# Kernel optimization log

Measured on AMD Instinct MI355X. Metric: run time of the kernel, lower is better.

Reference implementation:

```python
import jax, jax.numpy as jnp
import numpy as np

STRIDES = [(2, 2), (3, 3), (4, 4)]
EPS = 1e-5


def _conv1x1(x, w, b):
    # x: [B,C,H,W], w: [O,C] -> [B,O,H,W]
    return jnp.einsum('bchw,oc->bohw', x, w) + b[None, :, None, None]


def _stitch(x, hs, ws):
    # x: [B,dk,H,W] -> patches [B, hs*ws, dk*oh*ow]; patch index = i*ws + j matches
    # torch.stack over itertools.product(range(hs), range(ws)) of x[:,:,i::hs,j::ws]
    b, dk, H, W = x.shape
    oh, ow = H // hs, W // ws
    p = x.reshape(b, dk, oh, hs, ow, ws).transpose(0, 3, 5, 1, 2, 4)  # [B,hs,ws,dk,oh,ow]
    return p.reshape(b, hs * ws, dk * oh * ow)


def _unstitch(y, b, dk, hs, ws, oh, ow):
    # faithful to the torch permute(0,3,1,4,2,5): H is assembled as (hs, oh), W as (ws, ow)
    y = y.reshape(b, hs, ws, dk, oh, ow).transpose(0, 3, 1, 4, 2, 5)  # [B,dk,hs,oh,ws,ow]
    return y.reshape(b, dk, hs * oh, ws * ow)


def _attention(q, k, v):
    d = q.shape[-1]
    scores = jnp.einsum('bpd,bqd->bpq', q, k) / jnp.sqrt(jnp.asarray(d, q.dtype))
    p = jax.nn.softmax(scores, axis=-1)
    return jnp.einsum('bpq,bqd->bpd', p, v)


def _forward(x, wq, bq, wk, bk, wv, bv, w_out, b_out, gamma, beta):
    b, c, h, w = x.shape
    n = len(STRIDES)
    dk = c // n
    q = _conv1x1(x, wq, bq)
    k = _conv1x1(x, wk, bk)
    v = _conv1x1(x, wv, bv)
    outs = []
    for idx, (ws_, hs_) in enumerate(STRIDES):
        sl = slice(idx * dk, (idx + 1) * dk)
        oh, ow = h // hs_, w // ws_
        qp = _stitch(q[:, sl], hs_, ws_)
        kp = _stitch(k[:, sl], hs_, ws_)
        vp = _stitch(v[:, sl], hs_, ws_)
        y = _attention(qp, kp, vp)  # [B, hs*ws, dk*oh*ow]
        outs.append(_unstitch(y, b, dk, hs_, ws_, oh, ow))
    out = jnp.concatenate(outs, axis=1)  # [B,C,H,W]
    # output_linear: Conv3x3 -> BatchNorm2d (training-mode batch stats) -> LeakyReLU(0.2)
    y = jax.lax.conv_general_dilated(out, w_out, (1, 1), 'SAME',
                                     dimension_numbers=('NCHW', 'OIHW', 'NCHW'))
    y = y + b_out[None, :, None, None]
    mean = jnp.mean(y, axis=(0, 2, 3), keepdims=True)
    var = jnp.var(y, axis=(0, 2, 3), keepdims=True)
    y = (y - mean) * jax.lax.rsqrt(var + EPS)
    y = y * gamma[None, :, None, None] + beta[None, :, None, None]
    return jnp.where(y >= 0, y, 0.2 * y)


def setup_inputs() -> dict:
    key = jax.random.key(0)
    ks = jax.random.split(key, 10)
    B, C, H, W = 16, 192, 96, 96
    s = 0.02
    return {
        'x': jax.random.normal(ks[0], (B, C, H, W), jnp.float32),
        'wq': jax.random.normal(ks[1], (C, C), jnp.float32) * s,
        'bq': jnp.zeros((C,), jnp.float32),
        'wk': jax.random.normal(ks[2], (C, C), jnp.float32) * s,
        'bk': jnp.zeros((C,), jnp.float32),
        'wv': jax.random.normal(ks[3], (C, C), jnp.float32) * s,
        'bv': jnp.zeros((C,), jnp.float32),
        'w_out': jax.random.normal(ks[4], (C, C, 3, 3), jnp.float32) * s,
        'b_out': jnp.zeros((C,), jnp.float32),
        'gamma': jnp.ones((C,), jnp.float32),
        'beta': jnp.zeros((C,), jnp.float32),
    }


def reference(x, wq, bq, wk, bk, wv, bv, w_out, b_out, gamma, beta):
    return _forward(x, wq, bq, wk, bk, wv, bv, w_out, b_out, gamma, beta)
```

## Files before the change

### kernel.cpp

```cpp
#include <hip/hip_runtime.h>
#include <hip/hip_bf16.h>

#define BB 16
#define CC 192
#define HH 96
#define WWW 96
#define HWSZ 9216
#define DKC 64

typedef __hip_bfloat16 bf16;
typedef __attribute__((ext_vector_type(8))) short s8v;
typedef __attribute__((ext_vector_type(4))) float f32x4;

__device__ __forceinline__ float bf2f(unsigned short u) {
  union { unsigned int i; float f; } x; x.i = ((unsigned int)u) << 16; return x.f;
}
__device__ __forceinline__ unsigned short f2bf(float f) {
  union { __hip_bfloat16 h; unsigned short u; } c; c.h = __float2bfloat16(f); return c.u;
}

__global__ __launch_bounds__(256) void prep_w_kernel(const float* __restrict__ w_out,
                                                     unsigned short* __restrict__ wb9T) {
  int e = blockIdx.x * 256 + threadIdx.x;
  if (e >= 9 * CC * CC) return;
  int c = e % CC;
  int oc = (e / CC) % CC;
  int sh = e / (CC * CC);
  wb9T[e] = f2bf(w_out[((size_t)(oc * CC + c)) * 9 + sh]);
}

__global__ __launch_bounds__(256) void prep_wqkv_kernel(
    const float* __restrict__ wq, const float* __restrict__ wk, const float* __restrict__ wv,
    unsigned short* __restrict__ wqkv) {
  int e = blockIdx.x * 256 + threadIdx.x;
  if (e >= 3 * CC * CC) return;
  int sel = e / (CC * CC), r = e % (CC * CC);
  const float* w = sel == 0 ? wq : sel == 1 ? wk : wv;
  wqkv[e] = f2bf(w[r]);
}

__global__ __launch_bounds__(256) void xcvt_kernel(const float* __restrict__ x,
                                                   unsigned short* __restrict__ xb) {
  __shared__ float xt[CC][65];
  int b = blockIdx.x / 144, tile = blockIdx.x % 144;
  int pix0 = tile * 64;
  const float* xsrc = x + (size_t)b * CC * HWSZ + pix0;
  for (int e = threadIdx.x; e < CC * 16; e += 256) {
    int c = e >> 4, seg = e & 15;
    float4 t4 = *(const float4*)(xsrc + (size_t)c * HWSZ + seg * 4);
    xt[c][seg * 4 + 0] = t4.x; xt[c][seg * 4 + 1] = t4.y;
    xt[c][seg * 4 + 2] = t4.z; xt[c][seg * 4 + 3] = t4.w;
  }
  __syncthreads();
  unsigned short* dst = xb + ((size_t)(b * HWSZ + pix0)) * CC;
  for (int e = threadIdx.x; e < 24 * 64; e += 256) {
    int cg = e >> 6, p = e & 63;
    uint4 ov;
    unsigned short* ou = (unsigned short*)&ov;
    #pragma unroll
    for (int j = 0; j < 8; ++j) ou[j] = f2bf(xt[cg * 8 + j][p]);
    *(uint4*)(dst + (size_t)p * CC + cg * 8) = ov;
  }
}

#define VTS 232
__global__ __launch_bounds__(256) void qkv_mfma_kernel(
    const unsigned short* __restrict__ xb, const unsigned short* __restrict__ wqkv,
    const float* __restrict__ bq, const float* __restrict__ bk, const float* __restrict__ bv,
    unsigned short* __restrict__ q, unsigned short* __restrict__ k,
    unsigned short* __restrict__ v) {
  __shared__ unsigned short xl[96 * 200];
  __shared__ unsigned short vt[48 * VTS];
  const int tid = threadIdx.x;
  const int bid = (blockIdx.x & 7) * 192 + (blockIdx.x >> 3);
  const int h = bid % HH;
  const int b = bid / HH;
  const int lane = tid & 63, wid = tid >> 6;
  const int lr = lane & 15, hi8 = (lane >> 4) * 8, rowb = (lane >> 4) * 4;
  const int n0 = wid * 48;
  const unsigned short* xrow = xb + ((size_t)(b * HWSZ + h * WWW)) * CC;

  #pragma unroll
  for (int i = 0; i < 9; ++i) {
    int u = tid + i * 256;
    int pix = u / 24, cg = u % 24;
    *(uint4*)(xl + pix * 200 + cg * 8) = *(const uint4*)(xrow + (size_t)pix * CC + cg * 8);
  }
  __syncthreads();

  for (int sel = 0; sel < 3; ++sel) {
    const unsigned short* wsel = wqkv + (size_t)sel * CC * CC;
    f32x4 acc[6][3];
    #pragma unroll
    for (int mt = 0; mt < 6; ++mt)
      #pragma unroll
      for (int nt = 0; nt < 3; ++nt) acc[mt][nt] = (f32x4){0.f, 0.f, 0.f, 0.f};

    auto loadB = [&](int ck, s8v (&dst)[3]) {
      const unsigned short* src = wsel + ck * 32 + hi8;
      #pragma unroll
      for (int nt = 0; nt < 3; ++nt)
        dst[nt] = *(const s8v*)(src + (size_t)(n0 + nt * 16 + lr) * CC);
    };
    auto loadA = [&](int ck, s8v (&dst)[6]) {
      #pragma unroll
      for (int mt = 0; mt < 6; ++mt)
        dst[mt] = *(const s8v*)(xl + (mt * 16 + lr) * 200 + ck * 32 + hi8);
    };
    auto qstep = [&](int ck, s8v (&slot)[3], s8v (&acur)[6], s8v (&anxt)[6]) {
      if (ck < 5) loadA(ck + 1, anxt);
      #pragma unroll
      for (int mt = 0; mt < 6; ++mt)
        #pragma unroll
        for (int nt = 0; nt < 3; ++nt)
          acc[mt][nt] = __builtin_amdgcn_mfma_f32_16x16x32_bf16(acur[mt], slot[nt], acc[mt][nt], 0, 0, 0);
      if (ck + 3 < 6) loadB(ck + 3, slot);
    };

    s8v br0[3], br1[3], br2[3], aA[6], aB[6];
    loadB(0, br0); loadB(1, br1); loadB(2, br2);
    loadA(0, aA);
    qstep(0, br0, aA, aB);
    qstep(1, br1, aB, aA);
    qstep(2, br2, aA, aB);
    qstep(3, br0, aB, aA);
    qstep(4, br1, aA, aB);
    qstep(5, br2, aB, aA);

    const float* bsel = (sel == 0 ? bq : sel == 1 ? bk : bv);
    float bias[3];
    #pragma unroll
    for (int nt = 0; nt < 3; ++nt) bias[nt] = bsel[n0 + nt * 16 + lr];
    unsigned short* dst = (sel == 0 ? q : sel == 1 ? k : v) + ((size_t)(b * HWSZ + h * WWW)) * CC;
    #pragma unroll
    for (int pass = 0; pass < 2; ++pass) {
      __syncthreads();
      #pragma unroll
      for (int mt2 = 0; mt2 < 3; ++mt2)
        #pragma unroll
        for (int nt = 0; nt < 3; ++nt)
          #pragma unroll
          for (int i = 0; i < 4; ++i)
            vt[(mt2 * 16 + rowb + i) * VTS + n0 + nt * 16 + lr] =
                f2bf(acc[pass * 3 + mt2][nt][i] + bias[nt]);
      __syncthreads();
      for (int e = tid; e < 48 * 24; e += 256) {
        int p = e % 48, cg = e / 48;
        *(uint4*)(dst + (size_t)(pass * 48 + p) * CC + cg * 8) = *(uint4*)(vt + p * VTS + cg * 8);
      }
    }
  }
}

template <int HS, int WS, int OH, int OW, int IDX>
__global__ __launch_bounds__(256) void scores_kernel(
    const unsigned short* __restrict__ q, const unsigned short* __restrict__ k,
    float* __restrict__ scores) {
  constexpr int P = HS * WS;
  constexpr int PAIRS = P * P;
  constexpr int NB = 16;
  constexpr int NSUB = (256 / PAIRS) < 1 ? 1 : (256 / PAIRS);
  __shared__ float qt[128][P + 1];
  __shared__ float kt[128][P + 1];
  int b = blockIdx.x / NB;
  int blk = blockIdx.x % NB;
  const unsigned short* qb = q + (size_t)b * HWSZ * CC;
  const unsigned short* kb = k + (size_t)b * HWSZ * CC;
  int pr = threadIdx.x % PAIRS;
  int sub = threadIdx.x / PAIRS;
  int pi = pr / P, qi = pr % P;
  float acc = 0.f;
  for (int rs0 = blk * 2; rs0 < OH * OW; rs0 += NB * 2) {
    if (threadIdx.x < 16 * P) {
      int cg = threadIdx.x & 7;
      int t2 = threadIdx.x >> 3;
      int pp = t2 % P, rs2 = t2 / P;
      int rs = rs0 + rs2;
      int r = rs / OW, s = rs % OW;
      int i = pp / WS, j = pp % WS;
      int pixel = (r * HS + i) * WWW + s * WS + j;
      uint4 qv = *(const uint4*)(qb + (size_t)pixel * CC + IDX * 64 + cg * 8);
      uint4 kv = *(const uint4*)(kb + (size_t)pixel * CC + IDX * 64 + cg * 8);
      const unsigned short* qu = (const unsigned short*)&qv;
      const unsigned short* ku = (const unsigned short*)&kv;
      #pragma unroll
      for (int m = 0; m < 8; ++m) {
        qt[rs2 * 64 + cg * 8 + m][pp] = bf2f(qu[m]);
        kt[rs2 * 64 + cg * 8 + m][pp] = bf2f(ku[m]);
      }
    }
    __syncthreads();
    if (sub < NSUB) {
      #pragma unroll 4
      for (int pos = sub; pos < 128; pos += NSUB)
        acc += qt[pos][pi] * kt[pos][qi];
    }
    __syncthreads();
  }
  if (sub < NSUB) atomicAdd(scores + ((IDX * BB + b) * 256 + pr), acc);
}

__global__ void softmax_kernel(const float* __restrict__ scores, float* __restrict__ probs) {
  int t = threadIdx.x;
  int idx, b, p, P; float scale;
  if (t < 64)       { idx = 0; b = t >> 2;           p = t & 3;         P = 4;  scale = 1.f / 384.f; }
  else if (t < 208) { int u = t - 64;  idx = 1; b = u / 9;  p = u % 9;  P = 9;  scale = 1.f / 256.f; }
  else if (t < 464) { int u = t - 208; idx = 2; b = u >> 4; p = u & 15; P = 16; scale = 1.f / 192.f; }
  else return;
  const float* row = scores + (idx * BB + b) * 256 + p * P;
  float* orow = probs + (idx * BB + b) * 256 + p * P;
  float vals[16];
  float m = -1e30f;
  for (int i = 0; i < P; i++) { vals[i] = row[i] * scale; m = fmaxf(m, vals[i]); }
  float s = 0.f;
  for (int i = 0; i < P; i++) { vals[i] = expf(vals[i] - m); s += vals[i]; }
  float inv = 1.f / s;
  for (int i = 0; i < P; i++) orow[i] = vals[i] * inv;
}

template <int HS, int WS, int OH, int OW, int IDX>
__global__ __launch_bounds__(256) void pv_kernel(
    const unsigned short* __restrict__ v, const float* __restrict__ probs,
    unsigned short* __restrict__ attn) {
  constexpr int P = HS * WS;
  __shared__ unsigned short vl[HS * 96 * 72];
  __shared__ float pl[P * P];
  int b = blockIdx.x / OH;
  int r = blockIdx.x % OH;
  const int tid = threadIdx.x;
  for (int u = tid; u < HS * 96 * 8; u += 256) {
    int iq = u / 768, w = (u >> 3) % 96, cg = u & 7;
    *(uint4*)(vl + (iq * 96 + w) * 72 + cg * 8) =
        *(const uint4*)(v + ((size_t)(b * HWSZ + (r * HS + iq) * WWW + w)) * CC + IDX * 64 + cg * 8);
  }
  if (tid < P * P) pl[tid] = probs[(IDX * BB + b) * 256 + tid];
  __syncthreads();
  for (int u = tid; u < HS * 96 * 8; u += 256) {
    int i = u / 768, w = (u >> 3) % 96, cg = u & 7;
    int j = w / OW, s = w - j * OW;
    int p = i * WS + j;
    float acc[8];
    #pragma unroll
    for (int m = 0; m < 8; ++m) acc[m] = 0.f;
    #pragma unroll
    for (int iq = 0; iq < HS; ++iq) {
      #pragma unroll
      for (int jq = 0; jq < WS; ++jq) {
        float pw = pl[p * P + iq * WS + jq];
        s8v vv = *(const s8v*)(vl + (iq * 96 + s * WS + jq) * 72 + cg * 8);
        #pragma unroll
        for (int m = 0; m < 8; ++m) acc[m] += pw * bf2f((unsigned short)vv[m]);
      }
    }
    uint4 ov;
    ov.x = (unsigned int)f2bf(acc[0]) | ((unsigned int)f2bf(acc[1]) << 16);
    ov.y = (unsigned int)f2bf(acc[2]) | ((unsigned int)f2bf(acc[3]) << 16);
    ov.z = (unsigned int)f2bf(acc[4]) | ((unsigned int)f2bf(acc[5]) << 16);
    ov.w = (unsigned int)f2bf(acc[6]) | ((unsigned int)f2bf(acc[7]) << 16);
    *(uint4*)(attn + ((size_t)(b * HWSZ + (i * OH + r) * WWW + w)) * CC + IDX * 64 + cg * 8) = ov;
  }
}

__global__ __launch_bounds__(256) void conv_mfma_kernel(
    const unsigned short* __restrict__ attn, const unsigned short* __restrict__ wb9T,
    const float* __restrict__ b_out, unsigned short* __restrict__ ybf,
    float* __restrict__ bnsum, float* __restrict__ bnsqs) {
  __shared__ unsigned short al[3 * 98 * 40];
  const int tid = threadIdx.x;
  const int bid = (blockIdx.x & 7) * 192 + (blockIdx.x >> 3);
  const int h = bid % HH;
  const int b = bid / HH;
  const int lane = tid & 63, wid = tid >> 6;
  const int lr = lane & 15, hi8 = (lane >> 4) * 8, rowb = (lane >> 4) * 4;
  const int n0 = wid * 48;

  f32x4 acc[6][3];
  #pragma unroll
  for (int mt = 0; mt < 6; ++mt)
    #pragma unroll
    for (int nt = 0; nt < 3; ++nt) acc[mt][nt] = (f32x4){0.f, 0.f, 0.f, 0.f};

  uint4 aregs[5];
  auto stageA_LOAD = [&](int chunk) {
    int c0 = chunk * 32;
    #pragma unroll
    for (int i = 0; i < 5; ++i) {
      int u = tid + i * 256;
      if (u < 1176) {
        int row = u / 392, rem = u % 392, wx = rem >> 2, qq = rem & 3;
        int hr = h + row - 1, w = wx - 1;
        uint4 val = make_uint4(0u, 0u, 0u, 0u);
        if (hr >= 0 && hr < HH && w >= 0 && w < WWW)
          val = *(const uint4*)(attn + ((size_t)(b * HWSZ + hr * WWW + w)) * CC + c0 + qq * 8);
        aregs[i] = val;
      }
    }
  };
  auto stageA_WRITE = [&]() {
    #pragma unroll
    for (int i = 0; i < 5; ++i) {
      int u = tid + i * 256;
      if (u < 1176) {
        int row = u / 392, rem = u % 392, wx = rem >> 2, qq = rem & 3;
        *(uint4*)(al + (row * 98 + wx) * 40 + qq * 8) = aregs[i];
      }
    }
  };
  auto loadB = [&](int it2, s8v (&dst)[3]) {
    int chunk = it2 / 9, sh = it2 % 9;
    const unsigned short* src = wb9T + (size_t)sh * CC * CC + chunk * 32 + hi8;
    #pragma unroll
    for (int nt = 0; nt < 3; ++nt)
      dst[nt] = *(const s8v*)(src + (size_t)(n0 + nt * 16 + lr) * CC);
  };

  s8v br0[3], br1[3], br2[3];
  stageA_LOAD(0);
  stageA_WRITE();
  loadB(0, br0); loadB(1, br1); loadB(2, br2);
  __syncthreads();

  auto step = [&](int chunk, int sh, s8v (&slot)[3]) {
    if (sh == 0 && chunk < 5) stageA_LOAD(chunk + 1);
    int ky = sh / 3, kx = sh % 3;
    s8v a[6];
    #pragma unroll
    for (int mt = 0; mt < 6; ++mt)
      a[mt] = *(const s8v*)(al + (ky * 98 + mt * 16 + lr + kx) * 40 + hi8);
    #pragma unroll
    for (int mt = 0; mt < 6; ++mt)
      #pragma unroll
      for (int nt = 0; nt < 3; ++nt)
        acc[mt][nt] = __builtin_amdgcn_mfma_f32_16x16x32_bf16(a[mt], slot[nt], acc[mt][nt], 0, 0, 0);
    int it = chunk * 9 + sh;
    if (it + 3 < 54) loadB(it + 3, slot);
  };

  for (int chunk = 0; chunk < 6; ++chunk) {
    step(chunk, 0, br0);
    step(chunk, 1, br1);
    step(chunk, 2, br2);
    step(chunk, 3, br0);
    step(chunk, 4, br1);
    step(chunk, 5, br2);
    step(chunk, 6, br0);
    step(chunk, 7, br1);
    step(chunk, 8, br2);
    if (chunk < 5) {
      __syncthreads();
      stageA_WRITE();
      __syncthreads();
    }
  }

  #pragma unroll
  for (int nt = 0; nt < 3; ++nt) {
    int oc = n0 + nt * 16 + lr;
    float bias = b_out[oc];
    float s1 = 0.f, s2 = 0.f;
    #pragma unroll
    for (int mt = 0; mt < 6; ++mt) {
      float v0 = acc[mt][nt][0] + bias;
      float v1 = acc[mt][nt][1] + bias;
      float v2 = acc[mt][nt][2] + bias;
      float v3 = acc[mt][nt][3] + bias;
      s1 += v0 + v1 + v2 + v3;
      s2 += v0 * v0 + v1 * v1 + v2 * v2 + v3 * v3;
      uint2 pk;
      pk.x = (unsigned int)f2bf(v0) | ((unsigned int)f2bf(v1) << 16);
      pk.y = (unsigned int)f2bf(v2) | ((unsigned int)f2bf(v3) << 16);
      *(uint2*)(ybf + ((size_t)(b * CC + oc)) * HWSZ + h * WWW + mt * 16 + rowb) = pk;
    }
    s1 += __shfl_down(s1, 32);
    s1 += __shfl_down(s1, 16);
    s2 += __shfl_down(s2, 32);
    s2 += __shfl_down(s2, 16);
    if (lane < 16) {
      atomicAdd(bnsum + oc, s1);
      atomicAdd(bnsqs + oc, s2);
    }
  }
}

__global__ void bnfin_kernel(const float* __restrict__ bnsum, const float* __restrict__ bnsqs,
                             const float* __restrict__ gamma, const float* __restrict__ beta,
                             float* __restrict__ scale, float* __restrict__ shift) {
  int c = threadIdx.x;
  if (c >= CC) return;
  const float n = 16.f * 9216.f;
  float mean = bnsum[c] / n;
  float var = bnsqs[c] / n - mean * mean;
  float inv = rsqrtf(var + 1e-5f);
  float sc = gamma[c] * inv;
  scale[c] = sc;
  shift[c] = beta[c] - mean * sc;
}

__global__ __launch_bounds__(256) void bnapply_kernel(const unsigned short* __restrict__ ybf,
                                                      float* __restrict__ y,
                                                      const float* __restrict__ scale,
                                                      const float* __restrict__ shift) {
  const int total8 = BB * CC * HWSZ / 8;
  for (int e = blockIdx.x * 256 + threadIdx.x; e < total8; e += gridDim.x * 256) {
    uint4 t = ((const uint4*)ybf)[e];
    const unsigned short* u = (const unsigned short*)&t;
    int oc = (e / (HWSZ / 8)) % CC;
    float sc = scale[oc], sh = shift[oc];
    float4 o0, o1;
    float w;
    w = bf2f(u[0]) * sc + sh; o0.x = w >= 0.f ? w : 0.2f * w;
    w = bf2f(u[1]) * sc + sh; o0.y = w >= 0.f ? w : 0.2f * w;
    w = bf2f(u[2]) * sc + sh; o0.z = w >= 0.f ? w : 0.2f * w;
    w = bf2f(u[3]) * sc + sh; o0.w = w >= 0.f ? w : 0.2f * w;
    w = bf2f(u[4]) * sc + sh; o1.x = w >= 0.f ? w : 0.2f * w;
    w = bf2f(u[5]) * sc + sh; o1.y = w >= 0.f ? w : 0.2f * w;
    w = bf2f(u[6]) * sc + sh; o1.z = w >= 0.f ? w : 0.2f * w;
    w = bf2f(u[7]) * sc + sh; o1.w = w >= 0.f ? w : 0.2f * w;
    ((float4*)y)[e * 2] = o0;
    ((float4*)y)[e * 2 + 1] = o1;
  }
}

extern "C" void kernel_launch(void* const* d_in, const int* in_sizes, int n_in,
                              void* d_out, int out_size, void* d_ws, size_t ws_size,
                              hipStream_t stream) {
  const float* x     = (const float*)d_in[0];
  const float* wq    = (const float*)d_in[1];
  const float* bq    = (const float*)d_in[2];
  const float* wk    = (const float*)d_in[3];
  const float* bk    = (const float*)d_in[4];
  const float* wv    = (const float*)d_in[5];
  const float* bv    = (const float*)d_in[6];
  const float* w_out = (const float*)d_in[7];
  const float* b_out = (const float*)d_in[8];
  const float* gamma = (const float*)d_in[9];
  const float* beta  = (const float*)d_in[10];

  char* ws = (char*)d_ws;
  const size_t TB = (size_t)BB * CC * HWSZ * sizeof(bf16);
  unsigned short* q    = (unsigned short*)(ws);
  unsigned short* ybf  = q;
  unsigned short* k    = (unsigned short*)(ws + TB);
  unsigned short* v    = (unsigned short*)(ws + 2 * TB);
  unsigned short* attn = (unsigned short*)(ws + 3 * TB);
  unsigned short* xb   = attn;
  unsigned short* wb9T = (unsigned short*)(ws + 4 * TB);
  unsigned short* wqkv = (unsigned short*)(ws + 4 * TB + 663552);
  float* scores = (float*)(ws + 4 * TB + 663552 + 221184);
  float* bnsum  = scores + 3 * BB * 256;
  float* bnsqs  = bnsum + CC;
  float* probs  = bnsqs + CC;
  float* scale  = probs + 3 * BB * 256;
  float* shift  = scale + CC;
  float* y = (float*)d_out;

  hipMemsetAsync(scores, 0, 49152 + 2 * CC * 4, stream);

  prep_w_kernel<<<(9 * CC * CC + 255) / 256, 256, 0, stream>>>(w_out, wb9T);
  prep_wqkv_kernel<<<(3 * CC * CC + 255) / 256, 256, 0, stream>>>(wq, wk, wv, wqkv);

  xcvt_kernel<<<BB * 144, 256, 0, stream>>>(x, xb);
  qkv_mfma_kernel<<<BB * HH, 256, 0, stream>>>(xb, wqkv, bq, bk, bv, q, k, v);

  scores_kernel<2, 2, 48, 48, 0><<<BB * 16, 256, 0, stream>>>(q, k, scores);
  scores_kernel<3, 3, 32, 32, 1><<<BB * 16, 256, 0, stream>>>(q, k, scores);
  scores_kernel<4, 4, 24, 24, 2><<<BB * 16, 256, 0, stream>>>(q, k, scores);

  softmax_kernel<<<1, 512, 0, stream>>>(scores, probs);

  pv_kernel<2, 2, 48, 48, 0><<<BB * 48, 256, 0, stream>>>(v, probs, attn);
  pv_kernel<3, 3, 32, 32, 1><<<BB * 32, 256, 0, stream>>>(v, probs, attn);
  pv_kernel<4, 4, 24, 24, 2><<<BB * 24, 256, 0, stream>>>(v, probs, attn);

  conv_mfma_kernel<<<BB * HH, 256, 0, stream>>>(attn, wb9T, b_out, ybf, bnsum, bnsqs);

  bnfin_kernel<<<1, 256, 0, stream>>>(bnsum, bnsqs, gamma, beta, scale, shift);
  bnapply_kernel<<<2048, 256, 0, stream>>>(ybf, y, scale, shift);
}
```

Baseline: 495.7 us.

## Compute attention scores with MFMA bf16 instead of LDS scalar dot products

Replaces the scalar LDS-based QK^T score reduction with a per-wave MFMA 16x16x32 bf16 accumulation. Each wave loads patch rows straight from global memory into registers, with software prefetch of the next position. The grid grows to 64 slabs per batch so more blocks share the long reduction. The cost is wasted MFMA lanes when P<16 and more atomicAdds on the small scores buffer.

```diff
diff --git a/kernel.cpp b/kernel.cpp
--- a/kernel.cpp
+++ b/kernel.cpp
@@ -153,51 +153,63 @@
 }
 
 template <int HS, int WS, int OH, int OW, int IDX>
-__global__ __launch_bounds__(256) void scores_kernel(
+__global__ __launch_bounds__(256) void scores_mfma_kernel(
     const unsigned short* __restrict__ q, const unsigned short* __restrict__ k,
     float* __restrict__ scores) {
   constexpr int P = HS * WS;
-  constexpr int PAIRS = P * P;
-  constexpr int NB = 16;
-  constexpr int NSUB = (256 / PAIRS) < 1 ? 1 : (256 / PAIRS);
-  __shared__ float qt[128][P + 1];
-  __shared__ float kt[128][P + 1];
-  int b = blockIdx.x / NB;
-  int blk = blockIdx.x % NB;
-  const unsigned short* qb = q + (size_t)b * HWSZ * CC;
-  const unsigned short* kb = k + (size_t)b * HWSZ * CC;
-  int pr = threadIdx.x % PAIRS;
-  int sub = threadIdx.x / PAIRS;
-  int pi = pr / P, qi = pr % P;
-  float acc = 0.f;
-  for (int rs0 = blk * 2; rs0 < OH * OW; rs0 += NB * 2) {
-    if (threadIdx.x < 16 * P) {
-      int cg = threadIdx.x & 7;
-      int t2 = threadIdx.x >> 3;
-      int pp = t2 % P, rs2 = t2 / P;
-      int rs = rs0 + rs2;
-      int r = rs / OW, s = rs % OW;
-      int i = pp / WS, j = pp % WS;
-      int pixel = (r * HS + i) * WWW + s * WS + j;
-      uint4 qv = *(const uint4*)(qb + (size_t)pixel * CC + IDX * 64 + cg * 8);
-      uint4 kv = *(const uint4*)(kb + (size_t)pixel * CC + IDX * 64 + cg * 8);
-      const unsigned short* qu = (const unsigned short*)&qv;
-      const unsigned short* ku = (const unsigned short*)&kv;
-      #pragma unroll
-      for (int m = 0; m < 8; ++m) {
-        qt[rs2 * 64 + cg * 8 + m][pp] = bf2f(qu[m]);
-        kt[rs2 * 64 + cg * 8 + m][pp] = bf2f(ku[m]);
+  constexpr int NPOS = OH * OW;
+  constexpr int SLABS = 64;
+  constexpr int STRIDE = SLABS * 4;
+  const int slab = blockIdx.x % SLABS;
+  const int b = blockIdx.x / SLABS;
+  const int wid = threadIdx.x >> 6;
+  const int lane = threadIdx.x & 63;
+  const int lr = lane & 15, g8 = (lane >> 4) * 8;
+  const int p = (lr < P) ? lr : 0;
+  const int pixoff = (p / WS) * WWW + (p % WS);
+  const unsigned short* qb = q + (size_t)b * HWSZ * CC + IDX * 64 + g8;
+  const unsigned short* kb = k + (size_t)b * HWSZ * CC + IDX * 64 + g8;
+
+  f32x4 acc = (f32x4){0.f, 0.f, 0.f, 0.f};
+  int rs = slab * 4 + wid;
+  if (rs < NPOS) {
+    s8v aq0, aq1, bk0, bk1;
+    {
+      int r = rs / OW, s = rs - r * OW;
+      size_t pix = (size_t)(r * HS * WWW + s * WS + pixoff) * CC;
+      aq0 = *(const s8v*)(qb + pix);
+      aq1 = *(const s8v*)(qb + pix + 32);
+      bk0 = *(const s8v*)(kb + pix);
+      bk1 = *(const s8v*)(kb + pix + 32);
+    }
+    for (;;) {
+      int nrs = rs + STRIDE;
+      s8v nq0, nq1, nk0, nk1;
+      if (nrs < NPOS) {
+        int r = nrs / OW, s = nrs - r * OW;
+        size_t pix = (size_t)(r * HS * WWW + s * WS + pixoff) * CC;
+        nq0 = *(const s8v*)(qb + pix);
+        nq1 = *(const s8v*)(qb + pix + 32);
+        nk0 = *(const s8v*)(kb + pix);
+        nk1 = *(const s8v*)(kb + pix + 32);
       }
-    }
-    __syncthreads();
-    if (sub < NSUB) {
-      #pragma unroll 4
-      for (int pos = sub; pos < 128; pos += NSUB)
-        acc += qt[pos][pi] * kt[pos][qi];
-    }
-    __syncthreads();
-  }
-  if (sub < NSUB) atomicAdd(scores + ((IDX * BB + b) * 256 + pr), acc);
+      acc = __builtin_amdgcn_mfma_f32_16x16x32_bf16(aq0, bk0, acc, 0, 0, 0);
+      acc = __builtin_amdgcn_mfma_f32_16x16x32_bf16(aq1, bk1, acc, 0, 0, 0);
+      if (nrs >= NPOS) break;
+      aq0 = nq0; aq1 = nq1; bk0 = nk0; bk1 = nk1;
+      rs = nrs;
+    }
+  }
+  const int col = lane & 15;
+  const int row0 = (lane >> 4) * 4;
+  if (col < P) {
+    float* sc = scores + (IDX * BB + b) * 256;
+    #pragma unroll
+    for (int i = 0; i < 4; ++i) {
+      int row = row0 + i;
+      if (row < P) atomicAdd(sc + row * P + col, acc[i]);
+    }
+  }
 }
 
 __global__ void softmax_kernel(const float* __restrict__ scores, float* __restrict__ probs) {
@@ -462,9 +474,9 @@
   xcvt_kernel<<<BB * 144, 256, 0, stream>>>(x, xb);
   qkv_mfma_kernel<<<BB * HH, 256, 0, stream>>>(xb, wqkv, bq, bk, bv, q, k, v);
 
-  scores_kernel<2, 2, 48, 48, 0><<<BB * 16, 256, 0, stream>>>(q, k, scores);
-  scores_kernel<3, 3, 32, 32, 1><<<BB * 16, 256, 0, stream>>>(q, k, scores);
-  scores_kernel<4, 4, 24, 24, 2><<<BB * 16, 256, 0, stream>>>(q, k, scores);
+  scores_mfma_kernel<2, 2, 48, 48, 0><<<BB * 64, 256, 0, stream>>>(q, k, scores);
+  scores_mfma_kernel<3, 3, 32, 32, 1><<<BB * 64, 256, 0, stream>>>(q, k, scores);
+  scores_mfma_kernel<4, 4, 24, 24, 2><<<BB * 64, 256, 0, stream>>>(q, k, scores);
 
   softmax_kernel<<<1, 512, 0, stream>>>(scores, probs);
 
```

New measurement: 436.7 us (median of 2 runs). 11.9% less time.
